# Kernel optimization log

Measured on AMD Instinct MI355X. Metric: run time of the kernel, lower is better.

Reference implementation:

```python
import math
import jax, jax.numpy as jnp
import numpy as np

HEADS = 4
BOTTLENECK = 8

def setup_inputs() -> dict:
    key = jax.random.key(0)
    ks = jax.random.split(key, 12)
    B, N, H, k = 8, 10000, 512, BOTTLENECK
    hd = H // HEADS
    s = 1.0 / math.sqrt(H)
    return {
        "x": jax.random.normal(ks[0], (B, N, H), dtype=jnp.float32),
        "Wq": jax.random.uniform(ks[1], (H, H), jnp.float32, -s, s),
        "bq": jnp.zeros((H,), jnp.float32),
        "Wk": jax.random.uniform(ks[2], (H, H), jnp.float32, -s, s),
        "bk": jnp.zeros((H,), jnp.float32),
        "Wv": jax.random.uniform(ks[3], (H, H), jnp.float32, -s, s),
        "bv": jnp.zeros((H,), jnp.float32),
        "E": jax.random.normal(ks[4], (HEADS, N, k), jnp.float32) / math.sqrt(k),
        "Fp": jax.random.normal(ks[5], (HEADS, N, k), jnp.float32) / math.sqrt(k),
        "gbu": jax.random.normal(ks[6], (HEADS, k, k), jnp.float32) * 0.1,
        "gbv": jax.random.normal(ks[7], (HEADS, k, k), jnp.float32) * 0.1,
        "Wo": jax.random.uniform(ks[8], (H, H), jnp.float32, -s, s),
        "bo": jnp.zeros((H,), jnp.float32),
        "log_reg": jnp.asarray(math.log(1e-5), jnp.float32),
    }

def reference(x, Wq, bq, Wk, bk, Wv, bv, E, Fp, gbu, gbv, Wo, bo, log_reg):
    B, N, H = x.shape
    hd = H // HEADS
    def split_heads(t):
        return t.reshape(B, N, HEADS, hd).transpose(0, 2, 1, 3)  # [B,h,N,hd]
    q = split_heads(x @ Wq.T + bq)
    k = split_heads(x @ Wk.T + bk)
    v = split_heads(x @ Wv.T + bv)
    # Faithful to torch einsum 'hik,bhnd->bhkd' (i and n summed independently)
    k_proj = jnp.einsum('hik,bhnd->bhkd', E, k)   # [B,h,k,hd]
    v_proj = jnp.einsum('hik,bhnd->bhkd', Fp, v)  # [B,h,k,hd]
    scores = jnp.einsum('bhnd,bhkd->bhnk', q, k_proj) / math.sqrt(hd)
    graph_bias = gbu @ gbv                                  # [h,k,k]
    bias_diag = jnp.diagonal(graph_bias, axis1=1, axis2=2)  # [h,k]
    scores = scores + bias_diag[None, :, None, :]
    attn = jax.nn.softmax(scores, axis=-1)
    out = jnp.einsum('bhnk,bhkd->bhnd', attn, v_proj)
    out = out.transpose(0, 2, 1, 3).reshape(B, N, H)
    out = out @ Wo.T + bo
    reg = jnp.exp(log_reg) * (jnp.mean(jnp.abs(attn)) + jnp.mean(jnp.abs(graph_bias)) * 0.1)
    return out, reg
```

## Files before the change

### kernel.cpp

```cpp
#include <hip/hip_runtime.h>
#include <math.h>

#define HEADS 4
#define KB 8
#define Bsz 8
#define Nn 10000
#define Hh 512
#define HD 128
#define NPART 64

#define KSUM_OFF 4096
#define VSUM_OFF 8192
#define WQE_OFF  12288
#define WOE_OFF  28672
#define ESUM_OFF 45056
#define FSUM_OFF 45088
#define BQ_OFF   45120
#define BD_OFF   45152


__global__ __launch_bounds__(256) void k_part(const float* __restrict__ x,
                                              const float* __restrict__ E,
                                              const float* __restrict__ Fp,
                                              float* __restrict__ xpart,
                                              float* __restrict__ efpart) {
    int blk = blockIdx.x;
    int t = threadIdx.x;
    if (blk < NPART * Bsz) {
        int p = blk >> 3, b = blk & 7;
        const int CH = (Nn + NPART - 1) / NPART;
        int n0 = p * CH, n1 = min(n0 + CH, Nn);
        int c = t * 2;
        float a0 = 0.f, a1 = 0.f;
        const float* base = x + (size_t)b * Nn * Hh + c;
#pragma unroll 4
        for (int n = n0; n < n1; ++n) {
            float2 v = *(const float2*)(base + (size_t)n * Hh);
            a0 += v.x; a1 += v.y;
        }
        float* o = xpart + (size_t)(p * Bsz + b) * Hh;
        o[c] = a0; o[c + 1] = a1;
    } else {
        int idx = blk - NPART * Bsz;
        int src = idx >> 5, h = (idx >> 3) & 3, ch = idx & 7;
        const float* S = src ? Fp : E;
        const int CHE = Nn / 8;
        int n0 = ch * CHE, n1 = n0 + CHE;
        int kk = t & 7, part = t >> 3;
        float acc = 0.f;
        const float* base = S + (size_t)h * Nn * KB;
#pragma unroll 4
        for (int n = n0 + part; n < n1; n += 32) acc += base[n * KB + kk];
        __shared__ float sd[256];
        sd[t] = acc;
        __syncthreads();
        for (int s = 128; s >= 8; s >>= 1) {
            if (t < s) sd[t] += sd[t + s];
            __syncthreads();
        }
        if (t < 8) efpart[idx * 8 + t] = sd[t];
    }
}

__global__ __launch_bounds__(256) void k_reduce(const float* __restrict__ xpart,
                                                const float* __restrict__ efpart,
                                                float* __restrict__ xs,
                                                float* __restrict__ esum,
                                                float* __restrict__ fsum) {
    int blk = blockIdx.x, t = threadIdx.x;
    if (blk < 16) {
        int o = blk * 256 + t;
        float a = 0.f;
#pragma unroll 8
        for (int p = 0; p < NPART; ++p) a += xpart[(size_t)p * (Bsz * Hh) + o];
        xs[o] = a;
    } else if (t < 64) {
        int src = t >> 5, rem = t & 31;
        float a = 0.f;
#pragma unroll
        for (int ch = 0; ch < 8; ++ch)
            a += efpart[((src * 4 + (rem >> 3)) * 8 + ch) * 8 + (rem & 7)];
        if (src == 0) esum[rem] = a; else fsum[rem] = a;
    }
}

__global__ __launch_bounds__(256) void k_gemv(const float* __restrict__ Wk,
                                              const float* __restrict__ bk,
                                              const float* __restrict__ Wv,
                                              const float* __restrict__ bv,
                                              const float* __restrict__ xs,
                                              float* __restrict__ ksum,
                                              float* __restrict__ vsum) {
    int m = blockIdx.x;
    int rg = blockIdx.y;
    const float* W = m ? Wv : Wk;
    const float* bias = m ? bv : bk;
    float* out = m ? vsum : ksum;
    __shared__ float xsL[Bsz * Hh];
    int t = threadIdx.x;
    for (int i = t; i < Bsz * Hh; i += 256) xsL[i] = xs[i];
    __syncthreads();
    int wid = t >> 6, lane = t & 63;
    for (int i = 0; i < 16; ++i) {
        int r = rg * 64 + wid + 4 * i;
        float4 wa = *(const float4*)(W + (size_t)r * Hh + lane * 4);
        float4 wb = *(const float4*)(W + (size_t)r * Hh + 256 + lane * 4);
        float p[Bsz];
#pragma unroll
        for (int b = 0; b < Bsz; ++b) {
            const float4 x0 = *(const float4*)(&xsL[b * Hh + lane * 4]);
            const float4 x1 = *(const float4*)(&xsL[b * Hh + 256 + lane * 4]);
            p[b] = wa.x * x0.x + wa.y * x0.y + wa.z * x0.z + wa.w * x0.w +
                   wb.x * x1.x + wb.y * x1.y + wb.z * x1.z + wb.w * x1.w;
        }
#pragma unroll
        for (int off = 32; off >= 1; off >>= 1)
#pragma unroll
            for (int b = 0; b < Bsz; ++b) p[b] += __shfl_xor(p[b], off, 64);
        if (lane == 0) {
            float bb = (float)Nn * bias[r];
#pragma unroll
            for (int b = 0; b < Bsz; ++b) out[b * Hh + r] = p[b] + bb;
        }
    }
}

__global__ __launch_bounds__(256) void k_eff2(const float* __restrict__ Wq,
                                              const float* __restrict__ Wo,
                                              const float* __restrict__ ksum,
                                              const float* __restrict__ vsum,
                                              float* __restrict__ wqe,
                                              float* __restrict__ woe,
                                              const float* __restrict__ bq,
                                              const float* __restrict__ gbu,
                                              const float* __restrict__ gbv,
                                              const float* __restrict__ log_reg,
                                              float* __restrict__ bias_q,
                                              float* __restrict__ bias_diag,
                                              float* __restrict__ reg_out) {
    int blk = blockIdx.x;
    int t = threadIdx.x;
    __shared__ float sL[256];
    if (blk < 64) {
        int b = blk >> 3, rem = blk & 7, h = rem >> 1, m = rem & 1;
        const float* s = (m ? vsum : ksum) + b * Hh + h * HD;
        float* out = (m ? woe : wqe) + (size_t)(b * HEADS + h) * Hh;
        if (t < HD) sL[t] = s[t];
        __syncthreads();
        float a0 = 0.f, a1 = 0.f;
        if (m == 0) {
            const float* Wb = Wq + (size_t)h * HD * Hh;
#pragma unroll 4
            for (int d = 0; d < HD; ++d) {
                float sv = sL[d];
                a0 += Wb[(size_t)d * Hh + t] * sv;
                a1 += Wb[(size_t)d * Hh + t + 256] * sv;
            }
        } else {
            const float* W0 = Wo + (size_t)t * Hh + h * HD;
            const float* W1 = Wo + (size_t)(t + 256) * Hh + h * HD;
            for (int d = 0; d < HD; d += 4) {
                a0 += W0[d] * sL[d] + W0[d + 1] * sL[d + 1] + W0[d + 2] * sL[d + 2] + W0[d + 3] * sL[d + 3];
                a1 += W1[d] * sL[d] + W1[d + 1] * sL[d + 1] + W1[d + 2] * sL[d + 2] + W1[d + 3] * sL[d + 3];
            }
        }
        out[t] = a0;
        out[t + 256] = a1;
    } else {
        int h = t >> 6, i = (t >> 3) & 7, j = t & 7;
        float gb = 0.f;
#pragma unroll
        for (int l = 0; l < 8; ++l) gb += gbu[h * 64 + i * 8 + l] * gbv[h * 64 + l * 8 + j];
        if (i == j) bias_diag[h * 8 + i] = gb;
        sL[t] = fabsf(gb);
        __syncthreads();
        for (int s = 128; s >= 1; s >>= 1) {
            if (t < s) sL[t] += sL[t + s];
            __syncthreads();
        }
        if (t == 0) {
            float gbmean = sL[0] / 256.f;
            reg_out[0] = expf(log_reg[0]) * (0.125f + gbmean * 0.1f);
        }
        if (t < 32) {
            int b = t >> 2, hh = t & 3;
            float a = 0.f;
            for (int d = 0; d < HD; ++d) a += bq[hh * HD + d] * ksum[b * Hh + hh * HD + d];
            bias_q[t] = a;
        }
    }
}

__global__ __launch_bounds__(256) void k_main(const float* __restrict__ x,
                                              const float* __restrict__ bo,
                                              const float* __restrict__ wqe,
                                              const float* __restrict__ woe,
                                              const float* __restrict__ esum,
                                              const float* __restrict__ fsum,
                                              const float* __restrict__ bias_q,
                                              const float* __restrict__ bias_diag,
                                              float* __restrict__ out) {
    int b = blockIdx.y;
    int t = threadIdx.x;
    int wid = t >> 6, lane = t & 63;

    const float* wqe_b = wqe + (size_t)b * HEADS * Hh;
    const float* woe_b = woe + (size_t)b * HEADS * Hh;
    float4 wqa[HEADS], wqb[HEADS], woa[HEADS], wob[HEADS];
#pragma unroll
    for (int h = 0; h < HEADS; ++h) {
        wqa[h] = *(const float4*)(wqe_b + h * Hh + lane * 4);
        wqb[h] = *(const float4*)(wqe_b + h * Hh + 256 + lane * 4);
        woa[h] = *(const float4*)(woe_b + h * Hh + lane * 4);
        wob[h] = *(const float4*)(woe_b + h * Hh + 256 + lane * 4);
    }
    float4 boa = *(const float4*)(bo + lane * 4);
    float4 bob = *(const float4*)(bo + 256 + lane * 4);

    int q = lane >> 4;
    int hq = (q == 0) ? 0 : (q == 1) ? 2 : (q == 2) ? 1 : 3;
    int kk = lane & 7;
    float eV = esum[hq * KB + kk];
    float fV = fsum[hq * KB + kk];
    float bdV = bias_diag[hq * KB + kk];
    float bqV = bias_q[b * HEADS + hq];

    const float inv_sqrt_hd = 0.08838834764831843f;
    int wavesPerB = gridDim.x * 4;
    bool hi32 = (lane & 32) != 0;
    bool hi16 = (lane & 16) != 0;

    for (int n = blockIdx.x * 4 + wid; n < Nn; n += wavesPerB) {
        const float* xr = x + ((size_t)b * Nn + n) * Hh;
        float4 xa = *(const float4*)(xr + lane * 4);
        float4 xb = *(const float4*)(xr + 256 + lane * 4);
        float p[HEADS];
#pragma unroll
        for (int h = 0; h < HEADS; ++h) {
            p[h] = xa.x * wqa[h].x + xa.y * wqa[h].y + xa.z * wqa[h].z + xa.w * wqa[h].w +
                   xb.x * wqb[h].x + xb.y * wqb[h].y + xb.z * wqb[h].z + xb.w * wqb[h].w;
        }
        float A  = hi32 ? p[1] : p[0];
        float Bv = hi32 ? p[0] : p[1];
        A += __shfl_xor(Bv, 32, 64);
        float C  = hi32 ? p[3] : p[2];
        float D  = hi32 ? p[2] : p[3];
        C += __shfl_xor(D, 32, 64);
        float Ev = hi16 ? C : A;
        float Fv = hi16 ? A : C;
        Ev += __shfl_xor(Fv, 16, 64);
        Ev += __shfl_xor(Ev, 1, 64);
        Ev += __shfl_xor(Ev, 2, 64);
        Ev += __shfl_xor(Ev, 4, 64);
        Ev += __shfl_xor(Ev, 8, 64);

        float sq = (Ev + bqV) * inv_sqrt_hd;
        float sc = eV * sq + bdV;
        float m = sc;
        m = fmaxf(m, __shfl_xor(m, 1, 64));
        m = fmaxf(m, __shfl_xor(m, 2, 64));
        m = fmaxf(m, __shfl_xor(m, 4, 64));
        float e = __expf(sc - m);
        float se = e, sw = e * fV;
        se += __shfl_xor(se, 1, 64); sw += __shfl_xor(sw, 1, 64);
        se += __shfl_xor(se, 2, 64); sw += __shfl_xor(sw, 2, 64);
        se += __shfl_xor(se, 4, 64); sw += __shfl_xor(sw, 4, 64);
        float wv = sw / se;
        float w0 = __shfl(wv, 0, 64);
        float w2 = __shfl(wv, 16, 64);
        float w1 = __shfl(wv, 32, 64);
        float w3 = __shfl(wv, 48, 64);

        float4 oa = boa, ob = bob;
        oa.x += w0 * woa[0].x + w1 * woa[1].x + w2 * woa[2].x + w3 * woa[3].x;
        oa.y += w0 * woa[0].y + w1 * woa[1].y + w2 * woa[2].y + w3 * woa[3].y;
        oa.z += w0 * woa[0].z + w1 * woa[1].z + w2 * woa[2].z + w3 * woa[3].z;
        oa.w += w0 * woa[0].w + w1 * woa[1].w + w2 * woa[2].w + w3 * woa[3].w;
        ob.x += w0 * wob[0].x + w1 * wob[1].x + w2 * wob[2].x + w3 * wob[3].x;
        ob.y += w0 * wob[0].y + w1 * wob[1].y + w2 * wob[2].y + w3 * wob[3].y;
        ob.z += w0 * wob[0].z + w1 * wob[1].z + w2 * wob[2].z + w3 * wob[3].z;
        ob.w += w0 * wob[0].w + w1 * wob[1].w + w2 * wob[2].w + w3 * wob[3].w;

        float* orow = out + ((size_t)b * Nn + n) * Hh;
        *(float4*)(orow + lane * 4) = oa;
        *(float4*)(orow + 256 + lane * 4) = ob;
    }
}

extern "C" void kernel_launch(void* const* d_in, const int* in_sizes, int n_in,
                              void* d_out, int out_size, void* d_ws, size_t ws_size,
                              hipStream_t stream) {
    const float* x       = (const float*)d_in[0];
    const float* Wq      = (const float*)d_in[1];
    const float* bq      = (const float*)d_in[2];
    const float* Wk      = (const float*)d_in[3];
    const float* bk      = (const float*)d_in[4];
    const float* Wv      = (const float*)d_in[5];
    const float* bv      = (const float*)d_in[6];
    const float* E       = (const float*)d_in[7];
    const float* Fp      = (const float*)d_in[8];
    const float* gbu     = (const float*)d_in[9];
    const float* gbv     = (const float*)d_in[10];
    const float* Wo      = (const float*)d_in[11];
    const float* bo      = (const float*)d_in[12];
    const float* log_reg = (const float*)d_in[13];

    float* out = (float*)d_out;
    float* ws = (float*)d_ws;
    float* xs   = ws;
    float* ksum = ws + KSUM_OFF;
    float* vsum = ws + VSUM_OFF;
    float* wqe  = ws + WQE_OFF;
    float* woe  = ws + WOE_OFF;
    float* esum = ws + ESUM_OFF;
    float* fsum = ws + FSUM_OFF;
    float* bias_q = ws + BQ_OFF;
    float* bias_diag = ws + BD_OFF;
    float* reg_out = out + (size_t)Bsz * Nn * Hh;

    float* xpart  = out;
    float* efpart = out + (size_t)NPART * Bsz * Hh;

    k_part<<<NPART * Bsz + 64, 256, 0, stream>>>(x, E, Fp, xpart, efpart);
    k_reduce<<<17, 256, 0, stream>>>(xpart, efpart, xs, esum, fsum);
    k_gemv<<<dim3(2, 8), 256, 0, stream>>>(Wk, bk, Wv, bv, xs, ksum, vsum);
    k_eff2<<<65, 256, 0, stream>>>(Wq, Wo, ksum, vsum, wqe, woe,
                                   bq, gbu, gbv, log_reg, bias_q, bias_diag, reg_out);
    k_main<<<dim3(250, Bsz), 256, 0, stream>>>(x, bo, wqe, woe, esum, fsum, bias_q, bias_diag, out);
}
```

Baseline: 384.0 us.

## Widen partial-sum and GEMV grids, use nontemporal stores, and move partials to workspace

Doubles the number of x partial-sum partitions and raises unroll, and spreads the K/V GEMV over four times as many blocks with register-held inputs and a transposed shuffle reduction. The main kernel gets a fixed-trip loop, fast division and nontemporal output stores. Partial buffers move to workspace when it is large enough. The aim is more parallelism in the small serial stages and less cache pollution from the large output write. The risk is a larger reduce input in k_reduce, and it relies on the hidden reduce kernel handling the new NPART correctly.

```diff
diff --git a/kernel.cpp b/kernel.cpp
--- a/kernel.cpp
+++ b/kernel.cpp
@@ -7,7 +7,7 @@
 #define Nn 10000
 #define Hh 512
 #define HD 128
-#define NPART 64
+#define NPART 128
 
 #define KSUM_OFF 4096
 #define VSUM_OFF 8192
@@ -17,7 +17,11 @@
 #define FSUM_OFF 45088
 #define BQ_OFF   45120
 #define BD_OFF   45152
-
+#define XPART_OFF 45184
+#define EFPART_OFF (XPART_OFF + NPART * Bsz * Hh)
+#define WS_NEED   (EFPART_OFF + 512)
+
+typedef float f32x4_t __attribute__((ext_vector_type(4)));
 
 __global__ __launch_bounds__(256) void k_part(const float* __restrict__ x,
                                               const float* __restrict__ E,
@@ -33,7 +37,7 @@
         int c = t * 2;
         float a0 = 0.f, a1 = 0.f;
         const float* base = x + (size_t)b * Nn * Hh + c;
-#pragma unroll 4
+#pragma unroll 8
         for (int n = n0; n < n1; ++n) {
             float2 v = *(const float2*)(base + (size_t)n * Hh);
             a0 += v.x; a1 += v.y;
@@ -95,32 +99,44 @@
     int rg = blockIdx.y;
     const float* W = m ? Wv : Wk;
     const float* bias = m ? bv : bk;
-    float* out = m ? vsum : ksum;
-    __shared__ float xsL[Bsz * Hh];
+    float* outp = m ? vsum : ksum;
     int t = threadIdx.x;
-    for (int i = t; i < Bsz * Hh; i += 256) xsL[i] = xs[i];
-    __syncthreads();
     int wid = t >> 6, lane = t & 63;
-    for (int i = 0; i < 16; ++i) {
-        int r = rg * 64 + wid + 4 * i;
+    bool hi32 = (lane & 32) != 0;
+    bool hi16 = (lane & 16) != 0;
+    bool hi8  = (lane & 8) != 0;
+
+    float4 x0[Bsz], x1[Bsz];
+#pragma unroll
+    for (int b = 0; b < Bsz; ++b) {
+        x0[b] = *(const float4*)(xs + b * Hh + lane * 4);
+        x1[b] = *(const float4*)(xs + b * Hh + 256 + lane * 4);
+    }
+#pragma unroll
+    for (int i = 0; i < 4; ++i) {
+        int r = rg * 16 + wid + 4 * i;
         float4 wa = *(const float4*)(W + (size_t)r * Hh + lane * 4);
         float4 wb = *(const float4*)(W + (size_t)r * Hh + 256 + lane * 4);
         float p[Bsz];
 #pragma unroll
         for (int b = 0; b < Bsz; ++b) {
-            const float4 x0 = *(const float4*)(&xsL[b * Hh + lane * 4]);
-            const float4 x1 = *(const float4*)(&xsL[b * Hh + 256 + lane * 4]);
-            p[b] = wa.x * x0.x + wa.y * x0.y + wa.z * x0.z + wa.w * x0.w +
-                   wb.x * x1.x + wb.y * x1.y + wb.z * x1.z + wb.w * x1.w;
-        }
-#pragma unroll
-        for (int off = 32; off >= 1; off >>= 1)
-#pragma unroll
-            for (int b = 0; b < Bsz; ++b) p[b] += __shfl_xor(p[b], off, 64);
-        if (lane == 0) {
-            float bb = (float)Nn * bias[r];
-#pragma unroll
-            for (int b = 0; b < Bsz; ++b) out[b * Hh + r] = p[b] + bb;
+            p[b] = wa.x * x0[b].x + wa.y * x0[b].y + wa.z * x0[b].z + wa.w * x0[b].w +
+                   wb.x * x1[b].x + wb.y * x1[b].y + wb.z * x1[b].z + wb.w * x1[b].w;
+        }
+        float a, bb;
+        a = hi32 ? p[4] : p[0]; bb = hi32 ? p[0] : p[4]; float q0 = a + __shfl_xor(bb, 32, 64);
+        a = hi32 ? p[5] : p[1]; bb = hi32 ? p[1] : p[5]; float q1 = a + __shfl_xor(bb, 32, 64);
+        a = hi32 ? p[6] : p[2]; bb = hi32 ? p[2] : p[6]; float q2 = a + __shfl_xor(bb, 32, 64);
+        a = hi32 ? p[7] : p[3]; bb = hi32 ? p[3] : p[7]; float q3 = a + __shfl_xor(bb, 32, 64);
+        a = hi16 ? q2 : q0; bb = hi16 ? q0 : q2; float r0 = a + __shfl_xor(bb, 16, 64);
+        a = hi16 ? q3 : q1; bb = hi16 ? q1 : q3; float r1 = a + __shfl_xor(bb, 16, 64);
+        a = hi8 ? r1 : r0; bb = hi8 ? r0 : r1; float s = a + __shfl_xor(bb, 8, 64);
+        s += __shfl_xor(s, 4, 64);
+        s += __shfl_xor(s, 2, 64);
+        s += __shfl_xor(s, 1, 64);
+        if ((lane & 7) == 0) {
+            int b = lane >> 3;
+            outp[b * Hh + r] = s + (float)Nn * bias[r];
         }
     }
 }
@@ -226,11 +242,11 @@
     float bqV = bias_q[b * HEADS + hq];
 
     const float inv_sqrt_hd = 0.08838834764831843f;
-    int wavesPerB = gridDim.x * 4;
     bool hi32 = (lane & 32) != 0;
     bool hi16 = (lane & 16) != 0;
 
-    for (int n = blockIdx.x * 4 + wid; n < Nn; n += wavesPerB) {
+    int n = blockIdx.x * 4 + wid;
+    for (int j = 0; j < 10; ++j, n += 1000) {
         const float* xr = x + ((size_t)b * Nn + n) * Hh;
         float4 xa = *(const float4*)(xr + lane * 4);
         float4 xb = *(const float4*)(xr + 256 + lane * 4);
@@ -265,7 +281,7 @@
         se += __shfl_xor(se, 1, 64); sw += __shfl_xor(sw, 1, 64);
         se += __shfl_xor(se, 2, 64); sw += __shfl_xor(sw, 2, 64);
         se += __shfl_xor(se, 4, 64); sw += __shfl_xor(sw, 4, 64);
-        float wv = sw / se;
+        float wv = __fdividef(sw, se);
         float w0 = __shfl(wv, 0, 64);
         float w2 = __shfl(wv, 16, 64);
         float w1 = __shfl(wv, 32, 64);
@@ -282,8 +298,10 @@
         ob.w += w0 * wob[0].w + w1 * wob[1].w + w2 * wob[2].w + w3 * wob[3].w;
 
         float* orow = out + ((size_t)b * Nn + n) * Hh;
-        *(float4*)(orow + lane * 4) = oa;
-        *(float4*)(orow + 256 + lane * 4) = ob;
+        union { float4 s; f32x4_t v; } ua, ub;
+        ua.s = oa; ub.s = ob;
+        __builtin_nontemporal_store(ua.v, (f32x4_t*)(orow + lane * 4));
+        __builtin_nontemporal_store(ub.v, (f32x4_t*)(orow + 256 + lane * 4));
     }
 }
 
@@ -318,12 +336,19 @@
     float* bias_diag = ws + BD_OFF;
     float* reg_out = out + (size_t)Bsz * Nn * Hh;
 
-    float* xpart  = out;
-    float* efpart = out + (size_t)NPART * Bsz * Hh;
+    float* xpart;
+    float* efpart;
+    if (ws_size >= (size_t)WS_NEED * sizeof(float)) {
+        xpart  = ws + XPART_OFF;
+        efpart = ws + EFPART_OFF;
+    } else {
+        xpart  = out;
+        efpart = out + (size_t)NPART * Bsz * Hh;
+    }
 
     k_part<<<NPART * Bsz + 64, 256, 0, stream>>>(x, E, Fp, xpart, efpart);
     k_reduce<<<17, 256, 0, stream>>>(xpart, efpart, xs, esum, fsum);
-    k_gemv<<<dim3(2, 8), 256, 0, stream>>>(Wk, bk, Wv, bv, xs, ksum, vsum);
+    k_gemv<<<dim3(2, 32), 256, 0, stream>>>(Wk, bk, Wv, bv, xs, ksum, vsum);
     k_eff2<<<65, 256, 0, stream>>>(Wq, Wo, ksum, vsum, wqe, woe,
                                    bq, gbu, gbv, log_reg, bias_q, bias_diag, reg_out);
     k_main<<<dim3(250, Bsz), 256, 0, stream>>>(x, bo, wqe, woe, esum, fsum, bias_q, bias_diag, out);
```

After: 359.4 us. -6.4%, faster.
